# Performance work log

Hardware: AMD Instinct MI355X
Metric: run time of the kernel (lower is better)

## Reference

```python
import jax, jax.numpy as jnp
import numpy as np

B, S, H, L, D, DI = 4, 32, 8, 128, 512, 2048
EPS = 1e-6
TEMP = float(D) ** 0.5


def layer_norm(x, g, b):
    mu = jnp.mean(x, axis=-1, keepdims=True)
    var = jnp.mean((x - mu) ** 2, axis=-1, keepdims=True)
    return (x - mu) * jax.lax.rsqrt(var + EPS) * g + b


def setup_inputs() -> dict:
    key = jax.random.key(0)
    ks = jax.random.split(key, 8)
    x = jax.random.normal(ks[0], (B, S, L, D), jnp.float32)
    mask = jax.random.randint(ks[1], (B, S, L), 0, 2, jnp.int32)
    # learned params
    w = jax.random.normal(ks[2], (1, 1, H, L, D), jnp.float32) * (1.0 / np.sqrt(D))
    v_w = jax.random.normal(ks[3], (D, D), jnp.float32) * 0.02   # nn.Linear weight (out,in)
    ln_g = jnp.ones((D,), jnp.float32)
    ln_b = jnp.zeros((D,), jnp.float32)
    w1 = jax.random.normal(ks[4], (DI, D), jnp.float32) * 0.02
    b1 = jnp.zeros((DI,), jnp.float32)
    w2 = jax.random.normal(ks[5], (D, DI), jnp.float32) * 0.02
    b2 = jnp.zeros((D,), jnp.float32)
    fln_g = jnp.ones((D,), jnp.float32)
    fln_b = jnp.zeros((D,), jnp.float32)
    return {"x": x, "mask": mask, "w": w, "v_w": v_w, "ln_g": ln_g, "ln_b": ln_b,
            "w1": w1, "b1": b1, "w2": w2, "b2": b2, "fln_g": fln_g, "fln_b": fln_b}


def reference(x, mask, w, v_w, ln_g, ln_b, w1, b1, w2, b2, fln_g, fln_b):
    # attn logits: broadcast mul + reduce over d_model == einsum over d
    attn = jnp.einsum('bsld,hld->bshl', x, w[0, 0]) / TEMP           # (B,S,H,L)
    attn = jnp.where(mask[:, :, None, :] == 0, -1e9, attn)
    attn = jax.nn.softmax(attn, axis=-1)                              # dropout: eval mode
    v = jnp.einsum('bsld,ed->bsle', x, v_w)                           # Linear no bias: x @ W.T
    out = jnp.einsum('bsld,bshl->bshd', v, attn)                      # weighted sum readout
    out = layer_norm(out, ln_g, ln_b)
    # PositionwiseFeedForward with residual + LayerNorm
    h = jax.nn.relu(jnp.einsum('bshd,fd->bshf', out, w1) + b1)
    y = jnp.einsum('bshf,df->bshd', h, w2) + b2 + out
    y = layer_norm(y, fln_g, fln_b)
    return y, attn
```

## Files before the change

### kernel.cpp

```cpp
#include <hip/hip_runtime.h>
#include <hip/hip_bf16.h>

#define BB 4
#define SS 32
#define HH 8
#define LL 128
#define DD 512
#define DI 2048
#define EPSN 1e-6f
#define INV_TEMP 0.04419417382415922f

#define NLOGW_BLK 512
#define NCAST_GRAN ((DI*DD/4)*2 + (DD*DD/4))
#define NCAST_BLK (NCAST_GRAN / 256)

#define NROW (BB*SS*HH)
#define SLICE ((size_t)NROW * DD)

typedef __attribute__((ext_vector_type(8))) short short8;
typedef __attribute__((ext_vector_type(4))) float float4v;

static __device__ __forceinline__ unsigned short f2b(float f) {
  __hip_bfloat16 h = __float2bfloat16(f);
  return *(unsigned short*)&h;
}

static __device__ __forceinline__ size_t pk(int m, int k, int K) {
  return ((((size_t)(m >> 4) * (K >> 5) + (k >> 5)) * 4 + ((k >> 3) & 3)) * 16
          + (m & 15)) * 8 + (k & 7);
}

__global__ __launch_bounds__(256) void pre_kernel(
    const float* __restrict__ x, const int* __restrict__ mask,
    const float* __restrict__ w, const float* __restrict__ w1,
    const float* __restrict__ w2, const float* __restrict__ v_w,
    unsigned short* __restrict__ w1b, unsigned short* __restrict__ w2b,
    unsigned short* __restrict__ v_wb, float* __restrict__ logits) {
  int blk = blockIdx.x;
  if (blk < NLOGW_BLK) {
    int wv = threadIdx.x >> 6, lane = threadIdx.x & 63;
    int p   = blk * 4 + wv;
    int l   = p >> 4;
    int bsg = p & 15;

    float4 wr[HH][2];
#pragma unroll
    for (int h = 0; h < HH; ++h) {
      const float4* wp = (const float4*)(w + ((size_t)h * LL + l) * DD) + lane * 2;
      wr[h][0] = wp[0];
      wr[h][1] = wp[1];
    }

#pragma unroll 2
    for (int i = 0; i < 8; ++i) {
      int bs = bsg * 8 + i;
      const float4* xr = (const float4*)(x + ((size_t)bs * LL + l) * DD) + lane * 2;
      float4 x0 = xr[0], x1 = xr[1];
      float acc[HH];
#pragma unroll
      for (int h = 0; h < HH; ++h) {
        acc[h] = x0.x * wr[h][0].x + x0.y * wr[h][0].y +
                 x0.z * wr[h][0].z + x0.w * wr[h][0].w +
                 x1.x * wr[h][1].x + x1.y * wr[h][1].y +
                 x1.z * wr[h][1].z + x1.w * wr[h][1].w;
      }
#pragma unroll
      for (int off = 32; off > 0; off >>= 1) {
#pragma unroll
        for (int h = 0; h < HH; ++h) acc[h] += __shfl_xor(acc[h], off);
      }
      if (lane == 0) {
        int msk = mask[bs * LL + l];
#pragma unroll
        for (int h = 0; h < HH; ++h) {
          float lg = msk ? acc[h] * INV_TEMP : -1e9f;
          logits[((size_t)bs * HH + h) * LL + l] = lg;
        }
      }
    }
  } else {
    const int n1 = (DI * DD) / 4;
    const int n2 = n1;
    int i = (blk - NLOGW_BLK) * 256 + threadIdx.x;
    float4 v;
    unsigned short* dst;
    size_t base;
    if (i < n1) {
      v = ((const float4*)w1)[i];
      dst = w1b;
      base = pk(i >> 7, (i & 127) * 4, DD);
    } else if (i < n1 + n2) {
      int j = i - n1;
      v = ((const float4*)w2)[j];
      dst = w2b;
      base = pk(j >> 9, (j & 511) * 4, DI);
    } else {
      int j = i - n1 - n2;
      v = ((const float4*)v_w)[j];
      dst = v_wb;
      base = pk(j >> 7, (j & 127) * 4, DD);
    }
    dst[base + 0] = f2b(v.x);
    dst[base + 1] = f2b(v.y);
    dst[base + 2] = f2b(v.z);
    dst[base + 3] = f2b(v.w);
  }
}

__global__ __launch_bounds__(512) void xa_kernel(
    const float* __restrict__ x, const float* __restrict__ logits,
    float* __restrict__ attn_out, unsigned short* __restrict__ xab) {
  int bs = blockIdx.x >> 1, half = blockIdx.x & 1;
  int t = threadIdx.x, wv = t >> 6, lane = t & 63;

  __shared__ float sattn_t[LL][HH];
  __shared__ float sxa[2][HH][256];

  if (wv < 4) {
    for (int h = wv; h < HH; h += 4) {
      const float* lg = logits + ((size_t)bs * HH + h) * LL;
      float v0 = lg[lane], v1 = lg[lane + 64];
      float m = fmaxf(v0, v1);
#pragma unroll
      for (int off = 32; off > 0; off >>= 1) m = fmaxf(m, __shfl_xor(m, off));
      float e0 = __expf(v0 - m), e1 = __expf(v1 - m);
      float s = e0 + e1;
#pragma unroll
      for (int off = 32; off > 0; off >>= 1) s += __shfl_xor(s, off);
      float inv = 1.f / s;
      e0 *= inv; e1 *= inv;
      sattn_t[lane][h]      = e0;
      sattn_t[lane + 64][h] = e1;
      if (half == 0) {
        float* ao = attn_out + ((size_t)bs * HH + h) * LL;
        ao[lane]      = e0;
        ao[lane + 64] = e1;
      }
    }
  }
  __syncthreads();

  int col = t & 255, lseg = t >> 8;
  int e = half * 256 + col;
  const float* xb = x + (size_t)bs * LL * DD;
  float acc[HH];
#pragma unroll
  for (int h = 0; h < HH; ++h) acc[h] = 0.f;
  int l0 = lseg * 64;
  for (int l = l0; l < l0 + 64; ++l) {
    float xv = xb[(size_t)l * DD + e];
    float4 a0 = *(const float4*)&sattn_t[l][0];
    float4 a1 = *(const float4*)&sattn_t[l][4];
    acc[0] += a0.x * xv; acc[1] += a0.y * xv;
    acc[2] += a0.z * xv; acc[3] += a0.w * xv;
    acc[4] += a1.x * xv; acc[5] += a1.y * xv;
    acc[6] += a1.z * xv; acc[7] += a1.w * xv;
  }
#pragma unroll
  for (int h = 0; h < HH; ++h) sxa[lseg][h][col] = acc[h];
  __syncthreads();
  if (t < 256) {
#pragma unroll
    for (int h = 0; h < HH; ++h) {
      int m = bs * HH + h;
      xab[pk(m, e, DD)] = f2b(sxa[0][h][t] + sxa[1][h][t]);
    }
  }
}

__global__ __launch_bounds__(256) void gemm_v_kernel(
    const unsigned short* __restrict__ xab, const unsigned short* __restrict__ v_wb,
    float* __restrict__ vpart) {
  int blk = blockIdx.x;
  int nt = blk & 7, mt = (blk >> 3) & 15, kslice = blk >> 7;
  int wv = threadIdx.x >> 6, lane = threadIdx.x & 63;
  int lm = lane & 15, lq = lane >> 4;

  int m0 = mt * 64 + wv * 16;
  int n0 = nt * 64;
  const short8* A8 = (const short8*)xab + (size_t)(m0 >> 4) * 16 * 64;
  const short8* B8 = (const short8*)v_wb;

  float4v acc[4];
#pragma unroll
  for (int nf = 0; nf < 4; ++nf) acc[nf] = (float4v){0.f, 0.f, 0.f, 0.f};

#pragma unroll
  for (int ci = 0; ci < 4; ++ci) {
    int c = kslice * 4 + ci;
    short8 a = A8[(size_t)c * 64 + lane];
#pragma unroll
    for (int nf = 0; nf < 4; ++nf) {
      short8 b = B8[((size_t)((n0 >> 4) + nf) * 16 + c) * 64 + lane];
      acc[nf] = __builtin_amdgcn_mfma_f32_16x16x32_bf16(a, b, acc[nf], 0, 0, 0);
    }
  }

  float* outp = vpart + (size_t)kslice * SLICE;
#pragma unroll
  for (int nf = 0; nf < 4; ++nf) {
    int col = n0 + nf * 16 + lm;
#pragma unroll
    for (int r = 0; r < 4; ++r)
      outp[(size_t)(m0 + lq * 4 + r) * DD + col] = acc[nf][r];
  }
}

__global__ __launch_bounds__(256) void ln_mid_kernel(
    const float* __restrict__ vpart, const float* __restrict__ ln_g,
    const float* __restrict__ ln_b, float* __restrict__ o_ln,
    unsigned short* __restrict__ o_lnb) {
  int wv = threadIdx.x >> 6, lane = threadIdx.x & 63;
  int row = blockIdx.x * 4 + wv;

  const float* p0 = vpart + (size_t)row * DD;
  float vals[8];
  float sum = 0.f, sq = 0.f;
#pragma unroll
  for (int k = 0; k < 8; ++k) {
    int d = lane + 64 * k;
    float v = p0[d] + p0[SLICE + d] + p0[2 * SLICE + d] + p0[3 * SLICE + d];
    vals[k] = v;
    sum += v;
    sq += v * v;
  }
#pragma unroll
  for (int off = 32; off > 0; off >>= 1) {
    sum += __shfl_xor(sum, off);
    sq  += __shfl_xor(sq, off);
  }
  float mu  = sum * (1.f / DD);
  float var = sq * (1.f / DD) - mu * mu;
  float rs  = rsqrtf(var + EPSN);
  float* op = o_ln + (size_t)row * DD;
#pragma unroll
  for (int k = 0; k < 8; ++k) {
    int d = lane + 64 * k;
    float v = (vals[k] - mu) * rs * ln_g[d] + ln_b[d];
    op[d] = v;
    o_lnb[pk(row, d, DD)] = f2b(v);
  }
}

__global__ __launch_bounds__(256) void gemm1_kernel(
    const unsigned short* __restrict__ o_lnb, const unsigned short* __restrict__ w1b,
    const float* __restrict__ b1, unsigned short* __restrict__ h1b) {
  int blk = blockIdx.x;
  int nt = blk & 31, mt = blk >> 5;
  int wv = threadIdx.x >> 6, lane = threadIdx.x & 63;
  int lm = lane & 15, lq = lane >> 4;

  int m0 = mt * 64 + wv * 16;
  int n0 = nt * 64;
  const short8* A8 = (const short8*)o_lnb + (size_t)(m0 >> 4) * 16 * 64;
  const short8* B8 = (const short8*)w1b;

  float4v acc[4];
#pragma unroll
  for (int nf = 0; nf < 4; ++nf) acc[nf] = (float4v){0.f, 0.f, 0.f, 0.f};

#pragma unroll 4
  for (int c = 0; c < 16; ++c) {
    short8 a = A8[(size_t)c * 64 + lane];
#pragma unroll
    for (int nf = 0; nf < 4; ++nf) {
      short8 b = B8[((size_t)((n0 >> 4) + nf) * 16 + c) * 64 + lane];
      acc[nf] = __builtin_amdgcn_mfma_f32_16x16x32_bf16(a, b, acc[nf], 0, 0, 0);
    }
  }

#pragma unroll
  for (int nf = 0; nf < 4; ++nf) {
    int col = n0 + nf * 16 + lm;
    float bb = b1[col];
#pragma unroll
    for (int r = 0; r < 4; ++r) {
      int row = m0 + lq * 4 + r;
      h1b[pk(row, col, DI)] = f2b(fmaxf(acc[nf][r] + bb, 0.f));
    }
  }
}

__global__ __launch_bounds__(256) void gemm2_kernel(
    const unsigned short* __restrict__ h1b, const unsigned short* __restrict__ w2b,
    float* __restrict__ ypart) {
  int blk = blockIdx.x;
  int nt = blk & 7, mt = (blk >> 3) & 15, kslice = blk >> 7;
  int wv = threadIdx.x >> 6, lane = threadIdx.x & 63;
  int lm = lane & 15, lq = lane >> 4;

  int m0 = mt * 64 + wv * 16;
  int n0 = nt * 64;
  const short8* A8 = (const short8*)h1b + (size_t)(m0 >> 4) * 64 * 64;
  const short8* B8 = (const short8*)w2b;

  float4v acc[4];
#pragma unroll
  for (int nf = 0; nf < 4; ++nf) acc[nf] = (float4v){0.f, 0.f, 0.f, 0.f};

#pragma unroll 4
  for (int ci = 0; ci < 16; ++ci) {
    int c = kslice * 16 + ci;
    short8 a = A8[(size_t)c * 64 + lane];
#pragma unroll
    for (int nf = 0; nf < 4; ++nf) {
      short8 b = B8[((size_t)((n0 >> 4) + nf) * 64 + c) * 64 + lane];
      acc[nf] = __builtin_amdgcn_mfma_f32_16x16x32_bf16(a, b, acc[nf], 0, 0, 0);
    }
  }

  float* outp = ypart + (size_t)kslice * SLICE;
#pragma unroll
  for (int nf = 0; nf < 4; ++nf) {
    int col = n0 + nf * 16 + lm;
#pragma unroll
    for (int r = 0; r < 4; ++r)
      outp[(size_t)(m0 + lq * 4 + r) * DD + col] = acc[nf][r];
  }
}

__global__ __launch_bounds__(256) void ln_final_kernel(
    const float* __restrict__ ypart, const float* __restrict__ o_ln,
    const float* __restrict__ b2, const float* __restrict__ fln_g,
    const float* __restrict__ fln_b, float* __restrict__ y_out) {
  int wv = threadIdx.x >> 6, lane = threadIdx.x & 63;
  int row = blockIdx.x * 4 + wv;

  const float* p0 = ypart + (size_t)row * DD;
  const float* ol = o_ln + (size_t)row * DD;
  float vals[8];
  float sum = 0.f, sq = 0.f;
#pragma unroll
  for (int k = 0; k < 8; ++k) {
    int d = lane + 64 * k;
    float v = p0[d] + p0[SLICE + d] + p0[2 * SLICE + d] + p0[3 * SLICE + d] +
              b2[d] + ol[d];
    vals[k] = v;
    sum += v;
    sq += v * v;
  }
#pragma unroll
  for (int off = 32; off > 0; off >>= 1) {
    sum += __shfl_xor(sum, off);
    sq  += __shfl_xor(sq, off);
  }
  float mu  = sum * (1.f / DD);
  float var = sq * (1.f / DD) - mu * mu;
  float rs  = rsqrtf(var + EPSN);
  float* yo = y_out + (size_t)row * DD;
#pragma unroll
  for (int k = 0; k < 8; ++k) {
    int d = lane + 64 * k;
    yo[d] = (vals[k] - mu) * rs * fln_g[d] + fln_b[d];
  }
}

extern "C" void kernel_launch(void* const* d_in, const int* in_sizes, int n_in,
                              void* d_out, int out_size, void* d_ws, size_t ws_size,
                              hipStream_t stream) {
  const float* x     = (const float*)d_in[0];
  const int*   mask  = (const int*)d_in[1];
  const float* w     = (const float*)d_in[2];
  const float* v_w   = (const float*)d_in[3];
  const float* ln_g  = (const float*)d_in[4];
  const float* ln_b  = (const float*)d_in[5];
  const float* w1    = (const float*)d_in[6];
  const float* b1    = (const float*)d_in[7];
  const float* w2    = (const float*)d_in[8];
  const float* b2    = (const float*)d_in[9];
  const float* fln_g = (const float*)d_in[10];
  const float* fln_b = (const float*)d_in[11];

  float* y    = (float*)d_out;
  float* attn = y + (size_t)BB * SS * HH * DD;

  char* ws = (char*)d_ws;
  float*          o_ln   = (float*)(ws);
  unsigned short* o_lnb  = (unsigned short*)(ws + 2097152);
  unsigned short* w1b    = (unsigned short*)(ws + 3145728);
  unsigned short* w2b    = (unsigned short*)(ws + 5242880);
  unsigned short* h1b    = (unsigned short*)(ws + 7340032);
  float*          ypart  = (float*)(ws + 11534336);
  unsigned short* v_wb   = (unsigned short*)(ws + 19922944);
  unsigned short* xab    = (unsigned short*)(ws + 20447232);
  float*          vpart  = (float*)(ws + 21495808);
  float*          logits = (float*)(ws + 29884416);

  pre_kernel<<<NLOGW_BLK + NCAST_BLK, 256, 0, stream>>>(
      x, mask, w, w1, w2, v_w, w1b, w2b, v_wb, logits);
  xa_kernel<<<BB * SS * 2, 512, 0, stream>>>(x, logits, attn, xab);
  gemm_v_kernel<<<512, 256, 0, stream>>>(xab, v_wb, vpart);
  ln_mid_kernel<<<256, 256, 0, stream>>>(vpart, ln_g, ln_b, o_ln, o_lnb);
  gemm1_kernel<<<512, 256, 0, stream>>>(o_lnb, w1b, b1, h1b);
  gemm2_kernel<<<512, 256, 0, stream>>>(h1b, w2b, ypart);
  ln_final_kernel<<<256, 256, 0, stream>>>(ypart, o_ln, b2, fln_g, fln_b, y);
}
```

Baseline: 156.2 us.

## Fuse softmax readout, V projection, and mid LayerNorm into one kernel

Result: no change. 156.2 us (-0.1%).

```diff
diff --git a/kernel.cpp b/kernel.cpp
--- a/kernel.cpp
+++ b/kernel.cpp
@@ -16,6 +16,7 @@
 
 #define NROW (BB*SS*HH)
 #define SLICE ((size_t)NROW * DD)
+#define NAVL_BLK 64
 
 typedef __attribute__((ext_vector_type(8))) short short8;
 typedef __attribute__((ext_vector_type(4))) float float4v;
@@ -107,138 +108,139 @@
   }
 }
 
-__global__ __launch_bounds__(512) void xa_kernel(
+__global__ __launch_bounds__(512) void attn_v_ln_kernel(
     const float* __restrict__ x, const float* __restrict__ logits,
-    float* __restrict__ attn_out, unsigned short* __restrict__ xab) {
-  int bs = blockIdx.x >> 1, half = blockIdx.x & 1;
+    const unsigned short* __restrict__ v_wb, const float* __restrict__ ln_g,
+    const float* __restrict__ ln_b, float* __restrict__ attn_out,
+    float* __restrict__ o_ln, unsigned short* __restrict__ o_lnb) {
+  int blk = blockIdx.x;
   int t = threadIdx.x, wv = t >> 6, lane = t & 63;
-
-  __shared__ float sattn_t[LL][HH];
-  __shared__ float sxa[2][HH][256];
-
-  if (wv < 4) {
-    for (int h = wv; h < HH; h += 4) {
-      const float* lg = logits + ((size_t)bs * HH + h) * LL;
-      float v0 = lg[lane], v1 = lg[lane + 64];
-      float m = fmaxf(v0, v1);
-#pragma unroll
-      for (int off = 32; off > 0; off >>= 1) m = fmaxf(m, __shfl_xor(m, off));
-      float e0 = __expf(v0 - m), e1 = __expf(v1 - m);
-      float s = e0 + e1;
-#pragma unroll
-      for (int off = 32; off > 0; off >>= 1) s += __shfl_xor(s, off);
-      float inv = 1.f / s;
-      e0 *= inv; e1 *= inv;
-      sattn_t[lane][h]      = e0;
-      sattn_t[lane + 64][h] = e1;
-      if (half == 0) {
-        float* ao = attn_out + ((size_t)bs * HH + h) * LL;
-        ao[lane]      = e0;
-        ao[lane + 64] = e1;
-      }
-    }
+  int bs0 = blk * 2;
+
+  __shared__ __align__(16) float sattnT[LL][20];
+  __shared__ __align__(16) unsigned short apk[16 * DD];
+  __shared__ float wstat[8][16][2];
+  __shared__ float rstat[16][2];
+
+#pragma unroll
+  for (int rr = 0; rr < 2; ++rr) {
+    int r = wv * 2 + rr;
+    int bs = bs0 + (r >> 3), h = r & 7;
+    const float* lg = logits + ((size_t)bs * HH + h) * LL;
+    float v0 = lg[lane], v1 = lg[lane + 64];
+    float m = fmaxf(v0, v1);
+#pragma unroll
+    for (int off = 32; off > 0; off >>= 1) m = fmaxf(m, __shfl_xor(m, off));
+    float e0 = __expf(v0 - m), e1 = __expf(v1 - m);
+    float s = e0 + e1;
+#pragma unroll
+    for (int off = 32; off > 0; off >>= 1) s += __shfl_xor(s, off);
+    float inv = 1.f / s;
+    e0 *= inv; e1 *= inv;
+    sattnT[lane][r]      = e0;
+    sattnT[lane + 64][r] = e1;
+    float* ao = attn_out + ((size_t)bs * HH + h) * LL;
+    ao[lane]      = e0;
+    ao[lane + 64] = e1;
   }
   __syncthreads();
 
-  int col = t & 255, lseg = t >> 8;
-  int e = half * 256 + col;
-  const float* xb = x + (size_t)bs * LL * DD;
-  float acc[HH];
-#pragma unroll
-  for (int h = 0; h < HH; ++h) acc[h] = 0.f;
-  int l0 = lseg * 64;
-  for (int l = l0; l < l0 + 64; ++l) {
-    float xv = xb[(size_t)l * DD + e];
-    float4 a0 = *(const float4*)&sattn_t[l][0];
-    float4 a1 = *(const float4*)&sattn_t[l][4];
-    acc[0] += a0.x * xv; acc[1] += a0.y * xv;
-    acc[2] += a0.z * xv; acc[3] += a0.w * xv;
-    acc[4] += a1.x * xv; acc[5] += a1.y * xv;
-    acc[6] += a1.z * xv; acc[7] += a1.w * xv;
-  }
-#pragma unroll
-  for (int h = 0; h < HH; ++h) sxa[lseg][h][col] = acc[h];
+  {
+    int e = t;
+    const float* xb = x + (size_t)bs0 * LL * DD + e;
+    float acc[16];
+#pragma unroll
+    for (int m = 0; m < 16; ++m) acc[m] = 0.f;
+#pragma unroll 2
+    for (int l = 0; l < LL; l += 4) {
+      float xv0[4], xv1[4];
+#pragma unroll
+      for (int j = 0; j < 4; ++j) {
+        xv0[j] = xb[(size_t)(l + j) * DD];
+        xv1[j] = xb[(size_t)(LL + l + j) * DD];
+      }
+#pragma unroll
+      for (int j = 0; j < 4; ++j) {
+        float4 a0 = *(const float4*)&sattnT[l + j][0];
+        float4 a1 = *(const float4*)&sattnT[l + j][4];
+        float4 a2 = *(const float4*)&sattnT[l + j][8];
+        float4 a3 = *(const float4*)&sattnT[l + j][12];
+        acc[0]  += a0.x * xv0[j]; acc[1]  += a0.y * xv0[j];
+        acc[2]  += a0.z * xv0[j]; acc[3]  += a0.w * xv0[j];
+        acc[4]  += a1.x * xv0[j]; acc[5]  += a1.y * xv0[j];
+        acc[6]  += a1.z * xv0[j]; acc[7]  += a1.w * xv0[j];
+        acc[8]  += a2.x * xv1[j]; acc[9]  += a2.y * xv1[j];
+        acc[10] += a2.z * xv1[j]; acc[11] += a2.w * xv1[j];
+        acc[12] += a3.x * xv1[j]; acc[13] += a3.y * xv1[j];
+        acc[14] += a3.z * xv1[j]; acc[15] += a3.w * xv1[j];
+      }
+    }
+    unsigned base = ((e >> 5) * 4 + ((e >> 3) & 3)) * 128 + (e & 7);
+#pragma unroll
+    for (int m = 0; m < 16; ++m) apk[base + m * 8] = f2b(acc[m]);
+  }
   __syncthreads();
-  if (t < 256) {
-#pragma unroll
-    for (int h = 0; h < HH; ++h) {
-      int m = bs * HH + h;
-      xab[pk(m, e, DD)] = f2b(sxa[0][h][t] + sxa[1][h][t]);
-    }
-  }
-}
-
-__global__ __launch_bounds__(256) void gemm_v_kernel(
-    const unsigned short* __restrict__ xab, const unsigned short* __restrict__ v_wb,
-    float* __restrict__ vpart) {
-  int blk = blockIdx.x;
-  int nt = blk & 7, mt = (blk >> 3) & 15, kslice = blk >> 7;
-  int wv = threadIdx.x >> 6, lane = threadIdx.x & 63;
+
   int lm = lane & 15, lq = lane >> 4;
-
-  int m0 = mt * 64 + wv * 16;
-  int n0 = nt * 64;
-  const short8* A8 = (const short8*)xab + (size_t)(m0 >> 4) * 16 * 64;
+  int n0 = wv * 64;
+  const short8* A8 = (const short8*)apk;
   const short8* B8 = (const short8*)v_wb;
-
-  float4v acc[4];
-#pragma unroll
-  for (int nf = 0; nf < 4; ++nf) acc[nf] = (float4v){0.f, 0.f, 0.f, 0.f};
-
-#pragma unroll
-  for (int ci = 0; ci < 4; ++ci) {
-    int c = kslice * 4 + ci;
-    short8 a = A8[(size_t)c * 64 + lane];
+  float4v acc3[4];
+#pragma unroll
+  for (int nf = 0; nf < 4; ++nf) acc3[nf] = (float4v){0.f, 0.f, 0.f, 0.f};
+#pragma unroll 4
+  for (int c = 0; c < 16; ++c) {
+    short8 a = A8[c * 64 + lane];
 #pragma unroll
     for (int nf = 0; nf < 4; ++nf) {
       short8 b = B8[((size_t)((n0 >> 4) + nf) * 16 + c) * 64 + lane];
-      acc[nf] = __builtin_amdgcn_mfma_f32_16x16x32_bf16(a, b, acc[nf], 0, 0, 0);
-    }
-  }
-
-  float* outp = vpart + (size_t)kslice * SLICE;
+      acc3[nf] = __builtin_amdgcn_mfma_f32_16x16x32_bf16(a, b, acc3[nf], 0, 0, 0);
+    }
+  }
+
+  float srow[4], qrow[4];
+#pragma unroll
+  for (int r = 0; r < 4; ++r) {
+    float s = 0.f, q = 0.f;
+#pragma unroll
+    for (int nf = 0; nf < 4; ++nf) { float v = acc3[nf][r]; s += v; q += v * v; }
+#pragma unroll
+    for (int off = 1; off < 16; off <<= 1) {
+      s += __shfl_xor(s, off);
+      q += __shfl_xor(q, off);
+    }
+    srow[r] = s; qrow[r] = q;
+  }
+  if (lm == 0) {
+#pragma unroll
+    for (int r = 0; r < 4; ++r) {
+      wstat[wv][lq * 4 + r][0] = srow[r];
+      wstat[wv][lq * 4 + r][1] = qrow[r];
+    }
+  }
+  __syncthreads();
+  if (t < 16) {
+    float S = 0.f, Q = 0.f;
+#pragma unroll
+    for (int w8 = 0; w8 < 8; ++w8) { S += wstat[w8][t][0]; Q += wstat[w8][t][1]; }
+    float mu  = S * (1.f / DD);
+    float var = Q * (1.f / DD) - mu * mu;
+    rstat[t][0] = mu;
+    rstat[t][1] = rsqrtf(var + EPSN);
+  }
+  __syncthreads();
 #pragma unroll
   for (int nf = 0; nf < 4; ++nf) {
     int col = n0 + nf * 16 + lm;
-#pragma unroll
-    for (int r = 0; r < 4; ++r)
-      outp[(size_t)(m0 + lq * 4 + r) * DD + col] = acc[nf][r];
-  }
-}
-
-__global__ __launch_bounds__(256) void ln_mid_kernel(
-    const float* __restrict__ vpart, const float* __restrict__ ln_g,
-    const float* __restrict__ ln_b, float* __restrict__ o_ln,
-    unsigned short* __restrict__ o_lnb) {
-  int wv = threadIdx.x >> 6, lane = threadIdx.x & 63;
-  int row = blockIdx.x * 4 + wv;
-
-  const float* p0 = vpart + (size_t)row * DD;
-  float vals[8];
-  float sum = 0.f, sq = 0.f;
-#pragma unroll
-  for (int k = 0; k < 8; ++k) {
-    int d = lane + 64 * k;
-    float v = p0[d] + p0[SLICE + d] + p0[2 * SLICE + d] + p0[3 * SLICE + d];
-    vals[k] = v;
-    sum += v;
-    sq += v * v;
-  }
-#pragma unroll
-  for (int off = 32; off > 0; off >>= 1) {
-    sum += __shfl_xor(sum, off);
-    sq  += __shfl_xor(sq, off);
-  }
-  float mu  = sum * (1.f / DD);
-  float var = sq * (1.f / DD) - mu * mu;
-  float rs  = rsqrtf(var + EPSN);
-  float* op = o_ln + (size_t)row * DD;
-#pragma unroll
-  for (int k = 0; k < 8; ++k) {
-    int d = lane + 64 * k;
-    float v = (vals[k] - mu) * rs * ln_g[d] + ln_b[d];
-    op[d] = v;
-    o_lnb[pk(row, d, DD)] = f2b(v);
+    float g = ln_g[col], bcol = ln_b[col];
+#pragma unroll
+    for (int r = 0; r < 4; ++r) {
+      int row = lq * 4 + r;
+      float v = (acc3[nf][r] - rstat[row][0]) * rstat[row][1] * g + bcol;
+      int grow = blk * 16 + row;
+      o_ln[(size_t)grow * DD + col] = v;
+      o_lnb[pk(grow, col, DD)] = f2b(v);
+    }
   }
 }
 
@@ -382,15 +384,12 @@
   unsigned short* h1b    = (unsigned short*)(ws + 7340032);
   float*          ypart  = (float*)(ws + 11534336);
   unsigned short* v_wb   = (unsigned short*)(ws + 19922944);
-  unsigned short* xab    = (unsigned short*)(ws + 20447232);
-  float*          vpart  = (float*)(ws + 21495808);
   float*          logits = (float*)(ws + 29884416);
 
   pre_kernel<<<NLOGW_BLK + NCAST_BLK, 256, 0, stream>>>(
       x, mask, w, w1, w2, v_w, w1b, w2b, v_wb, logits);
-  xa_kernel<<<BB * SS * 2, 512, 0, stream>>>(x, logits, attn, xab);
-  gemm_v_kernel<<<512, 256, 0, stream>>>(xab, v_wb, vpart);
-  ln_mid_kernel<<<256, 256, 0, stream>>>(vpart, ln_g, ln_b, o_ln, o_lnb);
+  attn_v_ln_kernel<<<NAVL_BLK, 512, 0, stream>>>(
+      x, logits, v_wb, ln_g, ln_b, attn, o_ln, o_lnb);
   gemm1_kernel<<<512, 256, 0, stream>>>(o_lnb, w1b, b1, h1b);
   gemm2_kernel<<<512, 256, 0, stream>>>(h1b, w2b, ypart);
   ln_final_kernel<<<256, 256, 0, stream>>>(ypart, o_ln, b2, fln_g, fln_b, y);
```
